# Kernel tuning notes

Hardware: AMD Instinct MI355X
Metric: run time of the kernel (lower is better)

The kernel has to match this reference:

```python
import jax, jax.numpy as jnp
import numpy as np

EPS = 1e-5  # torch LayerNorm default eps
B, N, D_IN, E, H, V = 4096, 32, 256, 128, 512, 32

def _ln(x):
    # LayerNorm without affine (elementwise_affine=False), biased variance
    m = jnp.mean(x, axis=-1, keepdims=True)
    v = jnp.mean(jnp.square(x - m), axis=-1, keepdims=True)
    return (x - m) * jax.lax.rsqrt(v + EPS)

def _ln_gru_cell(x, h, i2h_W, i2h_b, h2h_W, h2h_b, hW_W, hW_b, hU_W, hU_b):
    gates = jax.nn.sigmoid(_ln(x @ i2h_W + i2h_b) + _ln(h @ h2h_W + h2h_b))  # [B,2H]
    hs = h.shape[-1]
    z_t = gates[:, :hs]
    r_t = gates[:, hs:]
    h_hat = jnp.tanh(_ln(x @ hW_W + hW_b) + r_t * _ln(h @ hU_W + hU_b))
    return (1.0 - z_t) * h + z_t * h_hat

def setup_inputs() -> dict:
    key = jax.random.key(0)
    ks = jax.random.split(key, 32)
    std0 = 1.0 / np.sqrt(H)
    u = lambda k, shp: jax.random.uniform(k, shp, jnp.float32, -std0, std0)
    in0 = 3 * E  # attn context + msg embedding + feedback embedding
    inp = {
        'sender_messages_embedded': jax.random.normal(ks[0], (B, E), jnp.float32),
        'prev_hidden': jax.random.normal(ks[1], (2, B, H), jnp.float32),
        'candidate_objects': jax.random.normal(ks[2], (B, N, D_IN), jnp.float32),
        'prev_msg_embedding': jax.random.normal(ks[3], (B, E), jnp.float32),
        # linear_objects_in_keys
        'Wk': jax.random.normal(ks[4], (D_IN, E), jnp.float32) * 0.05,
        'bk': jnp.zeros((E,), jnp.float32),
        # LayerNormGRUCell layer 0 (input 3E)
        'i2h_W0': u(ks[5], (in0, 2 * H)), 'i2h_b0': u(ks[6], (2 * H,)),
        'h2h_W0': u(ks[7], (H, 2 * H)), 'h2h_b0': u(ks[8], (2 * H,)),
        'hW_W0': u(ks[9], (in0, H)), 'hW_b0': u(ks[10], (H,)),
        'hU_W0': u(ks[11], (H, H)), 'hU_b0': u(ks[12], (H,)),
        # LayerNormGRUCell layer 1 (input H)
        'i2h_W1': u(ks[13], (H, 2 * H)), 'i2h_b1': u(ks[14], (2 * H,)),
        'h2h_W1': u(ks[15], (H, 2 * H)), 'h2h_b1': u(ks[16], (2 * H,)),
        'hW_W1': u(ks[17], (H, H)), 'hW_b1': u(ks[18], (H,)),
        'hU_W1': u(ks[19], (H, H)), 'hU_b1': u(ks[20], (H,)),
        # hidden_to_feedback_output
        'out_W': jax.random.normal(ks[21], (H, V), jnp.float32) * 0.05,
        'out_b': jnp.zeros((V,), jnp.float32),
    }
    return inp

def reference(sender_messages_embedded, prev_hidden, candidate_objects, prev_msg_embedding,
              Wk, bk,
              i2h_W0, i2h_b0, h2h_W0, h2h_b0, hW_W0, hW_b0, hU_W0, hU_b0,
              i2h_W1, i2h_b1, h2h_W1, h2h_b1, hW_W1, hW_b1, hU_W1, hU_b1,
              out_W, out_b):
    # object attention (dot): query = msg embedding, keys = projected candidates
    keys = candidate_objects @ Wk + bk                              # [B,N,E]
    scores = jnp.einsum('be,bne->bn', sender_messages_embedded, keys)
    weights = jax.nn.softmax(scores, axis=1)                        # [B,N]
    context = jnp.einsum('bn,bne->be', weights, keys)               # [B,E]
    rnn_input = jnp.concatenate([context, sender_messages_embedded, prev_msg_embedding], axis=-1)  # [B,3E]
    h0 = _ln_gru_cell(rnn_input, prev_hidden[0], i2h_W0, i2h_b0, h2h_W0, h2h_b0, hW_W0, hW_b0, hU_W0, hU_b0)
    h1 = _ln_gru_cell(h0, prev_hidden[1], i2h_W1, i2h_b1, h2h_W1, h2h_b1, hW_W1, hW_b1, hU_W1, hU_b1)
    logits = h1 @ out_W + out_b                                     # [B,V]
    logp = jax.nn.log_softmax(logits, axis=-1)
    probs = jnp.exp(logp)
    entropy = -jnp.sum(probs * logp, axis=-1)                       # [B]
    output_token = jnp.argmax(probs, axis=-1)                       # eval-mode argmax
    output_token_logits = jnp.take_along_axis(logp, output_token[:, None], axis=1)[:, 0]
    new_hidden = jnp.stack([h0, h1])                                # [2,B,H]
    return (output_token, entropy, output_token_logits, logits, new_hidden)
```

## Files before the change

### kernel.cpp

```cpp
#include <hip/hip_runtime.h>
#include <hip/hip_bf16.h>
#include <math.h>

#define B_SZ   4096
#define NCAND  32
#define DIN    256
#define E_SZ   128
#define H_SZ   512
#define VOCAB  32
#define LN_EPS 1e-5f

typedef unsigned short u16;
typedef unsigned int   u32;
typedef __attribute__((ext_vector_type(8))) short  short8;
typedef __attribute__((ext_vector_type(4))) float  floatx4;

static __device__ __forceinline__ float sigmoidf_(float x) {
    return 1.0f / (1.0f + expf(-x));
}
static __device__ __forceinline__ u16 f2bf(float x) {
    u32 u = __float_as_uint(x);
    return (u16)((u + 0x7FFFu + ((u >> 16) & 1u)) >> 16);
}
static __device__ __forceinline__ float bfbits2f(u16 h) {
    return __uint_as_float(((u32)h) << 16);
}

__global__ __launch_bounds__(256)
void transpose_split_w(const float* __restrict__ W1, const float* __restrict__ W2,
                       int N1, int N2, int K,
                       u16* __restrict__ Wt_hi, u16* __restrict__ Wt_lo)
{
    __shared__ float t[64][68];
    const int n0 = blockIdx.x * 64, k0 = blockIdx.y * 64;
    const int tid = threadIdx.x;

    {
        const int kl = tid >> 4, nl4 = (tid & 15) * 4;
        const int ng = n0 + nl4;
        const float* src; int col, ld;
        if (ng < N1) { src = W1; col = ng;      ld = N1; }
        else         { src = W2; col = ng - N1; ld = N2; }
        #pragma unroll
        for (int p = 0; p < 4; ++p) {
            float4 v = *(const float4*)(src + (size_t)(k0 + kl + p * 16) * ld + col);
            *(float4*)&t[kl + p * 16][nl4] = v;
        }
    }
    __syncthreads();

    const int nl = tid >> 2, kc = tid & 3;
    union { u16 us[16]; uint4 v[2]; } hb, lb;
    #pragma unroll
    for (int j = 0; j < 16; ++j) {
        float x = t[kc * 16 + j][nl];
        u16 h = f2bf(x);
        float r = x - bfbits2f(h);
        hb.us[j] = h;
        lb.us[j] = f2bf(r);
    }
    const size_t off = (size_t)(n0 + nl) * K + k0 + kc * 16;
    *(uint4*)(Wt_hi + off)     = hb.v[0];
    *(uint4*)(Wt_hi + off + 8) = hb.v[1];
    *(uint4*)(Wt_lo + off)     = lb.v[0];
    *(uint4*)(Wt_lo + off + 8) = lb.v[1];
}

__global__ __launch_bounds__(256)
void bias_cat_kernel(const float* __restrict__ b1, const float* __restrict__ b2,
                     int N1, int Ntot, float* __restrict__ out)
{
    int i = blockIdx.x * 256 + threadIdx.x;
    if (i < Ntot) out[i] = (i < N1) ? b1[i] : b2[i - N1];
}

__global__ __launch_bounds__(256)
void split_act_kernel(const float* __restrict__ src,
                      u16* __restrict__ hi, u16* __restrict__ lo, int n4)
{
    int i = blockIdx.x * 256 + threadIdx.x;
    if (i >= n4) return;
    float4 v = ((const float4*)src)[i];
    u16 h0 = f2bf(v.x), h1 = f2bf(v.y), h2 = f2bf(v.z), h3 = f2bf(v.w);
    u16 l0 = f2bf(v.x - bfbits2f(h0));
    u16 l1 = f2bf(v.y - bfbits2f(h1));
    u16 l2 = f2bf(v.z - bfbits2f(h2));
    u16 l3 = f2bf(v.w - bfbits2f(h3));
    uint2 hv, lv;
    hv.x = (u32)h0 | ((u32)h1 << 16); hv.y = (u32)h2 | ((u32)h3 << 16);
    lv.x = (u32)l0 | ((u32)l1 << 16); lv.y = (u32)l2 | ((u32)l3 << 16);
    ((uint2*)hi)[i] = hv;
    ((uint2*)lo)[i] = lv;
}

__global__ __launch_bounds__(256)
void mfma_gemm_kernel(const u16* __restrict__ Ah, const u16* __restrict__ Al,
                      const u16* __restrict__ Wth, const u16* __restrict__ Wtl,
                      const float* __restrict__ bias, float* __restrict__ C,
                      int M, int N, int K)
{
    __shared__ u16 sAh[128 * 40];
    __shared__ u16 sAl[128 * 40];
    __shared__ u16 sWh[128 * 40];
    __shared__ u16 sWl[128 * 40];

    const int tid  = threadIdx.x;
    const int lane = tid & 63;
    const int wave = tid >> 6;
    const int wm = (wave >> 1) * 64;
    const int wn = (wave & 1) * 64;
    const int r16 = lane & 15;
    const int q8  = (lane >> 4) * 8;

    const int m_base = blockIdx.y * 128;
    const int n_base = blockIdx.x * 128;

    const int row0 = tid >> 2,         col0 = (tid & 3) * 8;
    const int row1 = (tid + 256) >> 2, col1 = ((tid + 256) & 3) * 8;

    floatx4 acc[4][4] = {};

    for (int k0 = 0; k0 < K; k0 += 32) {
        {
            const size_t gA0 = (size_t)(m_base + row0) * K + k0 + col0;
            const size_t gA1 = (size_t)(m_base + row1) * K + k0 + col1;
            const size_t gW0 = (size_t)(n_base + row0) * K + k0 + col0;
            const size_t gW1 = (size_t)(n_base + row1) * K + k0 + col1;
            *(uint4*)&sAh[row0 * 40 + col0] = *(const uint4*)(Ah + gA0);
            *(uint4*)&sAh[row1 * 40 + col1] = *(const uint4*)(Ah + gA1);
            *(uint4*)&sAl[row0 * 40 + col0] = *(const uint4*)(Al + gA0);
            *(uint4*)&sAl[row1 * 40 + col1] = *(const uint4*)(Al + gA1);
            *(uint4*)&sWh[row0 * 40 + col0] = *(const uint4*)(Wth + gW0);
            *(uint4*)&sWh[row1 * 40 + col1] = *(const uint4*)(Wth + gW1);
            *(uint4*)&sWl[row0 * 40 + col0] = *(const uint4*)(Wtl + gW0);
            *(uint4*)&sWl[row1 * 40 + col1] = *(const uint4*)(Wtl + gW1);
        }
        __syncthreads();

        short8 ah[4], al[4], bh[4], bl[4];
        #pragma unroll
        for (int i = 0; i < 4; ++i) {
            const int ar = (wm + i * 16 + r16) * 40 + q8;
            ah[i] = *(const short8*)&sAh[ar];
            al[i] = *(const short8*)&sAl[ar];
            const int br = (wn + i * 16 + r16) * 40 + q8;
            bh[i] = *(const short8*)&sWh[br];
            bl[i] = *(const short8*)&sWl[br];
        }
        #pragma unroll
        for (int i = 0; i < 4; ++i)
            #pragma unroll
            for (int j = 0; j < 4; ++j) {
                acc[i][j] = __builtin_amdgcn_mfma_f32_16x16x32_bf16(ah[i], bh[j], acc[i][j], 0, 0, 0);
                acc[i][j] = __builtin_amdgcn_mfma_f32_16x16x32_bf16(ah[i], bl[j], acc[i][j], 0, 0, 0);
                acc[i][j] = __builtin_amdgcn_mfma_f32_16x16x32_bf16(al[i], bh[j], acc[i][j], 0, 0, 0);
            }
        __syncthreads();
    }

    const int quad = lane >> 4;
    #pragma unroll
    for (int j = 0; j < 4; ++j) {
        const int n = n_base + wn + j * 16 + r16;
        const float bv = bias[n];
        #pragma unroll
        for (int i = 0; i < 4; ++i) {
            #pragma unroll
            for (int r = 0; r < 4; ++r) {
                const int m = m_base + wm + i * 16 + quad * 4 + r;
                C[(size_t)m * N + n] = acc[i][j][r] + bv;
            }
        }
    }
}

__global__ __launch_bounds__(256)
void gemm_bt64_kernel(const float* __restrict__ A, const float* __restrict__ Bt,
                      float* __restrict__ C, int M, int N, int K, int ldc)
{
    __shared__ float As[16][68];
    __shared__ float Bs[16][68];

    const int tid = threadIdx.x;
    const int bm = blockIdx.y * 64;
    const int bn = blockIdx.x * 64;
    const int tx = tid & 15, ty = tid >> 4;
    const int m0 = ty * 4, n0 = tx * 4;
    const int arow = tid >> 2, acol = (tid & 3) * 4;

    float acc[4][4] = {};

    for (int k0 = 0; k0 < K; k0 += 16) {
        float4 a4 = *(const float4*)(A  + (size_t)(bm + arow) * K + (k0 + acol));
        float4 b4 = *(const float4*)(Bt + (size_t)(bn + arow) * K + (k0 + acol));
        As[acol + 0][arow] = a4.x; As[acol + 1][arow] = a4.y;
        As[acol + 2][arow] = a4.z; As[acol + 3][arow] = a4.w;
        Bs[acol + 0][arow] = b4.x; Bs[acol + 1][arow] = b4.y;
        Bs[acol + 2][arow] = b4.z; Bs[acol + 3][arow] = b4.w;
        __syncthreads();
        #pragma unroll
        for (int k = 0; k < 16; ++k) {
            float4 av = *(const float4*)&As[k][m0];
            float4 bv = *(const float4*)&Bs[k][n0];
            float aa[4] = {av.x, av.y, av.z, av.w};
            float bb[4] = {bv.x, bv.y, bv.z, bv.w};
            #pragma unroll
            for (int i = 0; i < 4; ++i)
                #pragma unroll
                for (int j = 0; j < 4; ++j)
                    acc[i][j] = fmaf(aa[i], bb[j], acc[i][j]);
        }
        __syncthreads();
    }

    #pragma unroll
    for (int i = 0; i < 4; ++i)
        *(float4*)(C + (size_t)(bm + m0 + i) * ldc + bn + n0) =
            make_float4(acc[i][0], acc[i][1], acc[i][2], acc[i][3]);
}

__global__ __launch_bounds__(256)
void attn_ctx_kernel(const float* __restrict__ co, const float* __restrict__ q,
                     const float* __restrict__ snd, const float* __restrict__ pmsg,
                     float* __restrict__ cbar, float* __restrict__ rnn_in)
{
    __shared__ float s_co[NCAND][264];
    __shared__ float s_q[DIN];
    __shared__ float s_scores[NCAND];
    __shared__ float s_w[NCAND];

    const int b   = blockIdx.x;
    const int tid = threadIdx.x;

    {
        const float4* cop = (const float4*)(co + (size_t)b * NCAND * DIN);
        #pragma unroll
        for (int i = 0; i < 8; ++i) {
            int idx = tid + i * 256;
            float4 v = cop[idx];
            *(float4*)&s_co[idx >> 6][(idx & 63) * 4] = v;
        }
        if (tid < DIN) s_q[tid] = q[(size_t)b * DIN + tid];
    }
    __syncthreads();

    {
        const int n = tid >> 3, part = tid & 7;
        float sc = 0.f;
        #pragma unroll
        for (int qq = 0; qq < 8; ++qq) {
            const int d = part * 4 + qq * 32;
            float4 cv = *(const float4*)&s_co[n][d];
            float4 qv = *(const float4*)&s_q[d];
            sc += cv.x * qv.x + cv.y * qv.y + cv.z * qv.z + cv.w * qv.w;
        }
        #pragma unroll
        for (int m = 4; m; m >>= 1) sc += __shfl_xor(sc, m);
        if (part == 0) s_scores[n] = sc;
    }
    __syncthreads();

    if (tid < NCAND) {
        float s  = s_scores[tid];
        float mx = s;
        #pragma unroll
        for (int m = 16; m; m >>= 1) mx = fmaxf(mx, __shfl_xor(mx, m));
        float e = expf(s - mx);
        float sum = e;
        #pragma unroll
        for (int m = 16; m; m >>= 1) sum += __shfl_xor(sum, m);
        s_w[tid] = e / sum;
    }
    __syncthreads();

    {
        float cb = 0.f;
        #pragma unroll
        for (int n = 0; n < NCAND; ++n) cb = fmaf(s_w[n], s_co[n][tid], cb);
        cbar[(size_t)b * DIN + tid] = cb;
    }
    if (tid < 128)
        rnn_in[(size_t)b * 384 + 128 + tid] = snd[(size_t)b * E_SZ + tid];
    else
        rnn_in[(size_t)b * 384 + 128 + tid] = pmsg[(size_t)b * E_SZ + (tid - 128)];
}

__global__ __launch_bounds__(256)
void gemm_ctx_kernel(const float* __restrict__ A, const float* __restrict__ Bm,
                     const float* __restrict__ bias, float* __restrict__ C,
                     int M, int N, int K, int ldc)
{
    __shared__ float As[16][132];
    __shared__ float Bs[16][68];

    const int tid = threadIdx.x;
    const int bm = blockIdx.y * 128;
    const int bn = blockIdx.x * 64;
    const int tx = tid & 15, ty = tid >> 4;
    const int m0 = ty * 8, n0 = tx * 4;
    const int arow = tid >> 1, acol = (tid & 1) * 8;
    const int brow = tid >> 4, bcol = (tid & 15) * 4;

    float acc[8][4] = {};

    for (int k0 = 0; k0 < K; k0 += 16) {
        float4 a0 = *(const float4*)(A + (size_t)(bm + arow) * K + (k0 + acol));
        float4 a1 = *(const float4*)(A + (size_t)(bm + arow) * K + (k0 + acol + 4));
        float4 b4 = *(const float4*)(Bm + (size_t)(k0 + brow) * N + (bn + bcol));
        As[acol + 0][arow] = a0.x; As[acol + 1][arow] = a0.y;
        As[acol + 2][arow] = a0.z; As[acol + 3][arow] = a0.w;
        As[acol + 4][arow] = a1.x; As[acol + 5][arow] = a1.y;
        As[acol + 6][arow] = a1.z; As[acol + 7][arow] = a1.w;
        *(float4*)&Bs[brow][bcol] = b4;
        __syncthreads();
        #pragma unroll
        for (int k = 0; k < 16; ++k) {
            float4 av0 = *(const float4*)&As[k][m0];
            float4 av1 = *(const float4*)&As[k][m0 + 4];
            float4 bv  = *(const float4*)&Bs[k][n0];
            float aa[8] = {av0.x, av0.y, av0.z, av0.w, av1.x, av1.y, av1.z, av1.w};
            float bb[4] = {bv.x, bv.y, bv.z, bv.w};
            #pragma unroll
            for (int i = 0; i < 8; ++i)
                #pragma unroll
                for (int j = 0; j < 4; ++j)
                    acc[i][j] = fmaf(aa[i], bb[j], acc[i][j]);
        }
        __syncthreads();
    }

    const float4 bv = *(const float4*)(bias + bn + n0);
    #pragma unroll
    for (int i = 0; i < 8; ++i) {
        float4 o;
        o.x = acc[i][0] + bv.x; o.y = acc[i][1] + bv.y;
        o.z = acc[i][2] + bv.z; o.w = acc[i][3] + bv.w;
        *(float4*)(C + (size_t)(bm + m0 + i) * ldc + bn + n0) = o;
    }
}

__global__ __launch_bounds__(256)
void gru_combine_kernel(const float* __restrict__ gxc, const float* __restrict__ ghc,
                        const float* __restrict__ hprev, float* __restrict__ hout)
{
    const int b    = blockIdx.x;
    const int tid  = threadIdx.x;
    const int lane = tid & 63, wv = tid >> 6;

    __shared__ float s_part[4][8];
    __shared__ float s_gates[1024];

    const float* gxb = gxc + (size_t)b * 1536;
    const float* ghb = ghc + (size_t)b * 1536;

    const float4 gx4 = *(const float4*)(gxb + tid * 4);
    const float4 gh4 = *(const float4*)(ghb + tid * 4);
    const float2 cx2 = *(const float2*)(gxb + 1024 + tid * 2);
    const float2 ch2 = *(const float2*)(ghb + 1024 + tid * 2);

    float v[8];
    v[0] = gx4.x + gx4.y + gx4.z + gx4.w;
    v[1] = gx4.x*gx4.x + gx4.y*gx4.y + gx4.z*gx4.z + gx4.w*gx4.w;
    v[2] = gh4.x + gh4.y + gh4.z + gh4.w;
    v[3] = gh4.x*gh4.x + gh4.y*gh4.y + gh4.z*gh4.z + gh4.w*gh4.w;
    v[4] = cx2.x + cx2.y;
    v[5] = cx2.x*cx2.x + cx2.y*cx2.y;
    v[6] = ch2.x + ch2.y;
    v[7] = ch2.x*ch2.x + ch2.y*ch2.y;

    #pragma unroll
    for (int i = 0; i < 8; ++i)
        #pragma unroll
        for (int m = 32; m; m >>= 1) v[i] += __shfl_xor(v[i], m);

    if (lane == 0) {
        #pragma unroll
        for (int i = 0; i < 8; ++i) s_part[wv][i] = v[i];
    }
    __syncthreads();

    float t[8];
    #pragma unroll
    for (int i = 0; i < 8; ++i)
        t[i] = s_part[0][i] + s_part[1][i] + s_part[2][i] + s_part[3][i];

    const float mgx = t[0] / 1024.f;
    const float rgx = 1.f / sqrtf(t[1] / 1024.f - mgx * mgx + LN_EPS);
    const float mgh = t[2] / 1024.f;
    const float rgh = 1.f / sqrtf(t[3] / 1024.f - mgh * mgh + LN_EPS);
    const float mcx = t[4] / 512.f;
    const float rcx = 1.f / sqrtf(t[5] / 512.f - mcx * mcx + LN_EPS);
    const float mch = t[6] / 512.f;
    const float rch = 1.f / sqrtf(t[7] / 512.f - mch * mch + LN_EPS);

    float4 g;
    g.x = sigmoidf_((gx4.x - mgx) * rgx + (gh4.x - mgh) * rgh);
    g.y = sigmoidf_((gx4.y - mgx) * rgx + (gh4.y - mgh) * rgh);
    g.z = sigmoidf_((gx4.z - mgx) * rgx + (gh4.z - mgh) * rgh);
    g.w = sigmoidf_((gx4.w - mgx) * rgx + (gh4.w - mgh) * rgh);
    *(float4*)&s_gates[tid * 4] = g;
    __syncthreads();

    const float2 hp2 = *(const float2*)(hprev + (size_t)b * 512 + tid * 2);
    const float z0 = s_gates[tid * 2 + 0];
    const float z1 = s_gates[tid * 2 + 1];
    const float r0 = s_gates[512 + tid * 2 + 0];
    const float r1 = s_gates[512 + tid * 2 + 1];

    const float hh0 = tanhf((cx2.x - mcx) * rcx + r0 * ((ch2.x - mch) * rch));
    const float hh1 = tanhf((cx2.y - mcx) * rcx + r1 * ((ch2.y - mch) * rch));
    const float hn0 = (1.f - z0) * hp2.x + z0 * hh0;
    const float hn1 = (1.f - z1) * hp2.y + z1 * hh1;

    *(float2*)(hout + (size_t)b * 512 + tid * 2) = make_float2(hn0, hn1);
}

__global__ __launch_bounds__(256)
void out_kernel(const float* __restrict__ h1, const float* __restrict__ W,
                const float* __restrict__ bias, float* __restrict__ out)
{
    __shared__ float s_h[4][512];
    const int wave = threadIdx.x >> 6, lane = threadIdx.x & 63;
    const int b = blockIdx.x * 4 + wave;

    {
        const float4* hp = (const float4*)(h1 + (size_t)b * 512);
        float4* sp = (float4*)&s_h[wave][0];
        sp[lane]      = hp[lane];
        sp[lane + 64] = hp[lane + 64];
    }
    __syncthreads();

    const int v = lane & 31, half = lane >> 5;
    float acc = 0.f;
    {
        const float* wp = W + (size_t)half * 256 * 32 + v;
        const float* hh = &s_h[wave][half * 256];
        for (int k = 0; k < 256; ++k) acc = fmaf(hh[k], wp[(size_t)k * 32], acc);
    }
    acc += __shfl_xor(acc, 32);
    const float logit = acc + bias[v];

    if (half == 0)
        out[(size_t)3 * B_SZ + (size_t)b * VOCAB + v] = logit;

    float mval = logit; int midx = v;
    #pragma unroll
    for (int m = 16; m; m >>= 1) {
        float ov = __shfl_xor(mval, m);
        int   oi = __shfl_xor(midx, m);
        if (ov > mval || (ov == mval && oi < midx)) { mval = ov; midx = oi; }
    }
    float ex = expf(logit - mval);
    float sum = ex;
    #pragma unroll
    for (int m = 16; m; m >>= 1) sum += __shfl_xor(sum, m);
    const float lse  = mval + logf(sum);
    const float logp = logit - lse;
    const float p    = expf(logp);
    float epl = p * logp;
    #pragma unroll
    for (int m = 16; m; m >>= 1) epl += __shfl_xor(epl, m);
    const float entropy = -epl;
    const float tok_logp = __shfl(logp, midx, 32);

    if (lane == 0) {
        out[b]             = (float)midx;
        out[B_SZ + b]      = entropy;
        out[2 * B_SZ + b]  = tok_logp;
    }
}

extern "C" void kernel_launch(void* const* d_in, const int* in_sizes, int n_in,
                              void* d_out, int out_size, void* d_ws, size_t ws_size,
                              hipStream_t stream)
{
    const float* snd    = (const float*)d_in[0];
    const float* ph     = (const float*)d_in[1];
    const float* co     = (const float*)d_in[2];
    const float* pmsg   = (const float*)d_in[3];
    const float* Wk     = (const float*)d_in[4];
    const float* bk     = (const float*)d_in[5];
    const float* i2hW0  = (const float*)d_in[6];
    const float* i2hb0  = (const float*)d_in[7];
    const float* h2hW0  = (const float*)d_in[8];
    const float* h2hb0  = (const float*)d_in[9];
    const float* hWW0   = (const float*)d_in[10];
    const float* hWb0   = (const float*)d_in[11];
    const float* hUW0   = (const float*)d_in[12];
    const float* hUb0   = (const float*)d_in[13];
    const float* i2hW1  = (const float*)d_in[14];
    const float* i2hb1  = (const float*)d_in[15];
    const float* h2hW1  = (const float*)d_in[16];
    const float* h2hb1  = (const float*)d_in[17];
    const float* hWW1   = (const float*)d_in[18];
    const float* hWb1   = (const float*)d_in[19];
    const float* hUW1   = (const float*)d_in[20];
    const float* hUb1   = (const float*)d_in[21];
    const float* outW   = (const float*)d_in[22];
    const float* outb   = (const float*)d_in[23];

    float* out = (float*)d_out;
    float* h0out = out + (size_t)3 * B_SZ + (size_t)B_SZ * VOCAB;
    float* h1out = h0out + (size_t)B_SZ * H_SZ;

    const float* h0prev = ph;
    const float* h1prev = ph + (size_t)B_SZ * H_SZ;

    char* p = (char*)d_ws;
    auto alloc_f = [&](size_t n) { float* r = (float*)p; p += n * 4; return r; };
    auto alloc_h = [&](size_t n) { u16* r = (u16*)p; p += ((n * 2 + 15) & ~15ull); return r; };

    float* qbuf   = alloc_f((size_t)B_SZ * 256);
    float* cbar   = alloc_f((size_t)B_SZ * 256);
    float* rnn_in = alloc_f((size_t)B_SZ * 384);
    float* gxc    = alloc_f((size_t)B_SZ * 1536);
    float* ghc    = alloc_f((size_t)B_SZ * 1536);
    u16* rin_hi = alloc_h((size_t)B_SZ * 384);
    u16* rin_lo = alloc_h((size_t)B_SZ * 384);
    u16* hp_hi  = alloc_h((size_t)2 * B_SZ * 512);
    u16* hp_lo  = alloc_h((size_t)2 * B_SZ * 512);
    u16* h0_hi  = alloc_h((size_t)B_SZ * 512);
    u16* h0_lo  = alloc_h((size_t)B_SZ * 512);
    u16* W0x_hi = alloc_h((size_t)1536 * 384);
    u16* W0x_lo = alloc_h((size_t)1536 * 384);
    u16* W0h_hi = alloc_h((size_t)1536 * 512);
    u16* W0h_lo = alloc_h((size_t)1536 * 512);
    u16* W1x_hi = alloc_h((size_t)1536 * 512);
    u16* W1x_lo = alloc_h((size_t)1536 * 512);
    u16* W1h_hi = alloc_h((size_t)1536 * 512);
    u16* W1h_lo = alloc_h((size_t)1536 * 512);
    float* b0x = alloc_f(1536);
    float* b0h = alloc_f(1536);
    float* b1x = alloc_f(1536);
    float* b1h = alloc_f(1536);

    transpose_split_w<<<dim3(24, 6), 256, 0, stream>>>(i2hW0, hWW0, 1024, 512, 384, W0x_hi, W0x_lo);
    transpose_split_w<<<dim3(24, 8), 256, 0, stream>>>(h2hW0, hUW0, 1024, 512, 512, W0h_hi, W0h_lo);
    transpose_split_w<<<dim3(24, 8), 256, 0, stream>>>(i2hW1, hWW1, 1024, 512, 512, W1x_hi, W1x_lo);
    transpose_split_w<<<dim3(24, 8), 256, 0, stream>>>(h2hW1, hUW1, 1024, 512, 512, W1h_hi, W1h_lo);
    bias_cat_kernel<<<6, 256, 0, stream>>>(i2hb0, hWb0, 1024, 1536, b0x);
    bias_cat_kernel<<<6, 256, 0, stream>>>(h2hb0, hUb0, 1024, 1536, b0h);
    bias_cat_kernel<<<6, 256, 0, stream>>>(i2hb1, hWb1, 1024, 1536, b1x);
    bias_cat_kernel<<<6, 256, 0, stream>>>(h2hb1, hUb1, 1024, 1536, b1h);
    split_act_kernel<<<(2 * B_SZ * 512 / 4 + 255) / 256, 256, 0, stream>>>(ph, hp_hi, hp_lo, 2 * B_SZ * 512 / 4);

    gemm_bt64_kernel<<<dim3(4, 64), 256, 0, stream>>>(snd, Wk, qbuf, B_SZ, 256, 128, 256);
    attn_ctx_kernel<<<B_SZ, 256, 0, stream>>>(co, qbuf, snd, pmsg, cbar, rnn_in);
    gemm_ctx_kernel<<<dim3(2, 32), 256, 0, stream>>>(cbar, Wk, bk, rnn_in, B_SZ, 128, 256, 384);
    split_act_kernel<<<(B_SZ * 384 / 4 + 255) / 256, 256, 0, stream>>>(rnn_in, rin_hi, rin_lo, B_SZ * 384 / 4);

    mfma_gemm_kernel<<<dim3(12, 32), 256, 0, stream>>>(rin_hi, rin_lo, W0x_hi, W0x_lo, b0x, gxc, B_SZ, 1536, 384);
    mfma_gemm_kernel<<<dim3(12, 32), 256, 0, stream>>>(hp_hi, hp_lo, W0h_hi, W0h_lo, b0h, ghc, B_SZ, 1536, 512);
    gru_combine_kernel<<<B_SZ, 256, 0, stream>>>(gxc, ghc, h0prev, h0out);
    split_act_kernel<<<(B_SZ * 512 / 4 + 255) / 256, 256, 0, stream>>>(h0out, h0_hi, h0_lo, B_SZ * 512 / 4);

    mfma_gemm_kernel<<<dim3(12, 32), 256, 0, stream>>>(h0_hi, h0_lo, W1x_hi, W1x_lo, b1x, gxc, B_SZ, 1536, 512);
    mfma_gemm_kernel<<<dim3(12, 32), 256, 0, stream>>>(hp_hi + (size_t)B_SZ * 512, hp_lo + (size_t)B_SZ * 512,
                                                      W1h_hi, W1h_lo, b1h, ghc, B_SZ, 1536, 512);
    gru_combine_kernel<<<B_SZ, 256, 0, stream>>>(gxc, ghc, h1prev, h1out);

    out_kernel<<<B_SZ / 4, 256, 0, stream>>>(h1out, outW, outb, out);
}
```

Before: 481.4 us.

## Fuse activation bf16 hi/lo split into GEMM loads and merge x/h GEMMs

The separate split_act passes that wrote bf16 hi/lo copies of activations are removed. The GEMM now reads fp32 activations and splits them into hi/lo while staging into shared memory. The x-side and h-side GEMMs of each GRU layer run as one launch with a doubled grid, selected by blockIdx.y. This cuts extra global round trips and launches and raises per-launch parallelism, but repeats the conversion work in every n-tile block and reads 2x more A bytes per tile.

```diff
diff --git a/kernel.cpp b/kernel.cpp
--- a/kernel.cpp
+++ b/kernel.cpp
@@ -26,6 +26,24 @@
     return __uint_as_float(((u32)h) << 16);
 }
 
+static __device__ __forceinline__ void split_store8(const float* __restrict__ g,
+                                                    u16* __restrict__ sh,
+                                                    u16* __restrict__ sl)
+{
+    float4 a = *(const float4*)g;
+    float4 b = *(const float4*)(g + 4);
+    float v[8] = {a.x, a.y, a.z, a.w, b.x, b.y, b.z, b.w};
+    union { u16 us[8]; uint4 q; } hb, lb;
+    #pragma unroll
+    for (int j = 0; j < 8; ++j) {
+        u16 h = f2bf(v[j]);
+        hb.us[j] = h;
+        lb.us[j] = f2bf(v[j] - bfbits2f(h));
+    }
+    *(uint4*)sh = hb.q;
+    *(uint4*)sl = lb.q;
+}
+
 __global__ __launch_bounds__(256)
 void transpose_split_w(const float* __restrict__ W1, const float* __restrict__ W2,
                        int N1, int N2, int K,
@@ -75,29 +93,12 @@
 }
 
 __global__ __launch_bounds__(256)
-void split_act_kernel(const float* __restrict__ src,
-                      u16* __restrict__ hi, u16* __restrict__ lo, int n4)
-{
-    int i = blockIdx.x * 256 + threadIdx.x;
-    if (i >= n4) return;
-    float4 v = ((const float4*)src)[i];
-    u16 h0 = f2bf(v.x), h1 = f2bf(v.y), h2 = f2bf(v.z), h3 = f2bf(v.w);
-    u16 l0 = f2bf(v.x - bfbits2f(h0));
-    u16 l1 = f2bf(v.y - bfbits2f(h1));
-    u16 l2 = f2bf(v.z - bfbits2f(h2));
-    u16 l3 = f2bf(v.w - bfbits2f(h3));
-    uint2 hv, lv;
-    hv.x = (u32)h0 | ((u32)h1 << 16); hv.y = (u32)h2 | ((u32)h3 << 16);
-    lv.x = (u32)l0 | ((u32)l1 << 16); lv.y = (u32)l2 | ((u32)l3 << 16);
-    ((uint2*)hi)[i] = hv;
-    ((uint2*)lo)[i] = lv;
-}
-
-__global__ __launch_bounds__(256)
-void mfma_gemm_kernel(const u16* __restrict__ Ah, const u16* __restrict__ Al,
-                      const u16* __restrict__ Wth, const u16* __restrict__ Wtl,
-                      const float* __restrict__ bias, float* __restrict__ C,
-                      int M, int N, int K)
+void mfma_gemm_dual_kernel(const float* __restrict__ Ax, const u16* __restrict__ Wxh,
+                           const u16* __restrict__ Wxl, const float* __restrict__ bx,
+                           float* __restrict__ Cx, int Kx,
+                           const float* __restrict__ Ahp, const u16* __restrict__ Whh,
+                           const u16* __restrict__ Whl, const float* __restrict__ bh,
+                           float* __restrict__ Ch, int Kh)
 {
     __shared__ u16 sAh[128 * 40];
     __shared__ u16 sAl[128 * 40];
@@ -112,8 +113,16 @@
     const int r16 = lane & 15;
     const int q8  = (lane >> 4) * 8;
 
-    const int m_base = blockIdx.y * 128;
+    const int sel    = blockIdx.y >> 5;
+    const int m_base = (blockIdx.y & 31) * 128;
     const int n_base = blockIdx.x * 128;
+
+    const float* A    = sel ? Ahp : Ax;
+    const u16*   Wth  = sel ? Whh : Wxh;
+    const u16*   Wtl  = sel ? Whl : Wxl;
+    const float* bias = sel ? bh  : bx;
+    float*       C    = sel ? Ch  : Cx;
+    const int    K    = sel ? Kh  : Kx;
 
     const int row0 = tid >> 2,         col0 = (tid & 3) * 8;
     const int row1 = (tid + 256) >> 2, col1 = ((tid + 256) & 3) * 8;
@@ -122,14 +131,12 @@
 
     for (int k0 = 0; k0 < K; k0 += 32) {
         {
-            const size_t gA0 = (size_t)(m_base + row0) * K + k0 + col0;
-            const size_t gA1 = (size_t)(m_base + row1) * K + k0 + col1;
+            split_store8(A + (size_t)(m_base + row0) * K + k0 + col0,
+                         &sAh[row0 * 40 + col0], &sAl[row0 * 40 + col0]);
+            split_store8(A + (size_t)(m_base + row1) * K + k0 + col1,
+                         &sAh[row1 * 40 + col1], &sAl[row1 * 40 + col1]);
             const size_t gW0 = (size_t)(n_base + row0) * K + k0 + col0;
             const size_t gW1 = (size_t)(n_base + row1) * K + k0 + col1;
-            *(uint4*)&sAh[row0 * 40 + col0] = *(const uint4*)(Ah + gA0);
-            *(uint4*)&sAh[row1 * 40 + col1] = *(const uint4*)(Ah + gA1);
-            *(uint4*)&sAl[row0 * 40 + col0] = *(const uint4*)(Al + gA0);
-            *(uint4*)&sAl[row1 * 40 + col1] = *(const uint4*)(Al + gA1);
             *(uint4*)&sWh[row0 * 40 + col0] = *(const uint4*)(Wth + gW0);
             *(uint4*)&sWh[row1 * 40 + col1] = *(const uint4*)(Wth + gW1);
             *(uint4*)&sWl[row0 * 40 + col0] = *(const uint4*)(Wtl + gW0);
@@ -137,23 +144,23 @@
         }
         __syncthreads();
 
-        short8 ah[4], al[4], bh[4], bl[4];
+        short8 ah[4], al[4], bhf[4], blf[4];
         #pragma unroll
         for (int i = 0; i < 4; ++i) {
             const int ar = (wm + i * 16 + r16) * 40 + q8;
             ah[i] = *(const short8*)&sAh[ar];
             al[i] = *(const short8*)&sAl[ar];
             const int br = (wn + i * 16 + r16) * 40 + q8;
-            bh[i] = *(const short8*)&sWh[br];
-            bl[i] = *(const short8*)&sWl[br];
+            bhf[i] = *(const short8*)&sWh[br];
+            blf[i] = *(const short8*)&sWl[br];
         }
         #pragma unroll
         for (int i = 0; i < 4; ++i)
             #pragma unroll
             for (int j = 0; j < 4; ++j) {
-                acc[i][j] = __builtin_amdgcn_mfma_f32_16x16x32_bf16(ah[i], bh[j], acc[i][j], 0, 0, 0);
-                acc[i][j] = __builtin_amdgcn_mfma_f32_16x16x32_bf16(ah[i], bl[j], acc[i][j], 0, 0, 0);
-                acc[i][j] = __builtin_amdgcn_mfma_f32_16x16x32_bf16(al[i], bh[j], acc[i][j], 0, 0, 0);
+                acc[i][j] = __builtin_amdgcn_mfma_f32_16x16x32_bf16(ah[i], bhf[j], acc[i][j], 0, 0, 0);
+                acc[i][j] = __builtin_amdgcn_mfma_f32_16x16x32_bf16(ah[i], blf[j], acc[i][j], 0, 0, 0);
+                acc[i][j] = __builtin_amdgcn_mfma_f32_16x16x32_bf16(al[i], bhf[j], acc[i][j], 0, 0, 0);
             }
         __syncthreads();
     }
@@ -168,7 +175,7 @@
             #pragma unroll
             for (int r = 0; r < 4; ++r) {
                 const int m = m_base + wm + i * 16 + quad * 4 + r;
-                C[(size_t)m * N + n] = acc[i][j][r] + bv;
+                C[(size_t)m * 1536 + n] = acc[i][j][r] + bv;
             }
         }
     }
@@ -516,12 +523,6 @@
     float* rnn_in = alloc_f((size_t)B_SZ * 384);
     float* gxc    = alloc_f((size_t)B_SZ * 1536);
     float* ghc    = alloc_f((size_t)B_SZ * 1536);
-    u16* rin_hi = alloc_h((size_t)B_SZ * 384);
-    u16* rin_lo = alloc_h((size_t)B_SZ * 384);
-    u16* hp_hi  = alloc_h((size_t)2 * B_SZ * 512);
-    u16* hp_lo  = alloc_h((size_t)2 * B_SZ * 512);
-    u16* h0_hi  = alloc_h((size_t)B_SZ * 512);
-    u16* h0_lo  = alloc_h((size_t)B_SZ * 512);
     u16* W0x_hi = alloc_h((size_t)1536 * 384);
     u16* W0x_lo = alloc_h((size_t)1536 * 384);
     u16* W0h_hi = alloc_h((size_t)1536 * 512);
@@ -543,21 +544,19 @@
     bias_cat_kernel<<<6, 256, 0, stream>>>(h2hb0, hUb0, 1024, 1536, b0h);
     bias_cat_kernel<<<6, 256, 0, stream>>>(i2hb1, hWb1, 1024, 1536, b1x);
     bias_cat_kernel<<<6, 256, 0, stream>>>(h2hb1, hUb1, 1024, 1536, b1h);
-    split_act_kernel<<<(2 * B_SZ * 512 / 4 + 255) / 256, 256, 0, stream>>>(ph, hp_hi, hp_lo, 2 * B_SZ * 512 / 4);
 
     gemm_bt64_kernel<<<dim3(4, 64), 256, 0, stream>>>(snd, Wk, qbuf, B_SZ, 256, 128, 256);
     attn_ctx_kernel<<<B_SZ, 256, 0, stream>>>(co, qbuf, snd, pmsg, cbar, rnn_in);
     gemm_ctx_kernel<<<dim3(2, 32), 256, 0, stream>>>(cbar, Wk, bk, rnn_in, B_SZ, 128, 256, 384);
-    split_act_kernel<<<(B_SZ * 384 / 4 + 255) / 256, 256, 0, stream>>>(rnn_in, rin_hi, rin_lo, B_SZ * 384 / 4);
-
-    mfma_gemm_kernel<<<dim3(12, 32), 256, 0, stream>>>(rin_hi, rin_lo, W0x_hi, W0x_lo, b0x, gxc, B_SZ, 1536, 384);
-    mfma_gemm_kernel<<<dim3(12, 32), 256, 0, stream>>>(hp_hi, hp_lo, W0h_hi, W0h_lo, b0h, ghc, B_SZ, 1536, 512);
+
+    mfma_gemm_dual_kernel<<<dim3(12, 64), 256, 0, stream>>>(
+        rnn_in, W0x_hi, W0x_lo, b0x, gxc, 384,
+        ph,     W0h_hi, W0h_lo, b0h, ghc, 512);
     gru_combine_kernel<<<B_SZ, 256, 0, stream>>>(gxc, ghc, h0prev, h0out);
-    split_act_kernel<<<(B_SZ * 512 / 4 + 255) / 256, 256, 0, stream>>>(h0out, h0_hi, h0_lo, B_SZ * 512 / 4);
-
-    mfma_gemm_kernel<<<dim3(12, 32), 256, 0, stream>>>(h0_hi, h0_lo, W1x_hi, W1x_lo, b1x, gxc, B_SZ, 1536, 512);
-    mfma_gemm_kernel<<<dim3(12, 32), 256, 0, stream>>>(hp_hi + (size_t)B_SZ * 512, hp_lo + (size_t)B_SZ * 512,
-                                                      W1h_hi, W1h_lo, b1h, ghc, B_SZ, 1536, 512);
+
+    mfma_gemm_dual_kernel<<<dim3(12, 64), 256, 0, stream>>>(
+        h0out,                    W1x_hi, W1x_lo, b1x, gxc, 512,
+        ph + (size_t)B_SZ * 512,  W1h_hi, W1h_lo, b1h, ghc, 512);
     gru_combine_kernel<<<B_SZ, 256, 0, stream>>>(gxc, ghc, h1prev, h1out);
 
     out_kernel<<<B_SZ / 4, 256, 0, stream>>>(h1out, outW, outb, out);
```

New measurement: 468.8 us. 2.6% less time.
